# Kernel optimization log

Hardware: AMD Instinct MI355X
Metric: run time of the kernel (lower is better)

## Reference

```python
import jax, jax.numpy as jnp
import numpy as np

NEG = -1e9  # masked_fill value from the original
B, S, E, H, L, V, CTX = 4, 1024, 1024, 16, 12, 50257, 1024
D = E // H
PAD_IDX = 0


def layernorm(x, g, b, eps=1e-5):
    m = jnp.mean(x, axis=-1, keepdims=True)
    v = jnp.var(x, axis=-1, keepdims=True)
    return (x - m) * jax.lax.rsqrt(v + eps) * g + b


def setup_inputs() -> dict:
    key = jax.random.key(0)
    ks = jax.random.split(key, 8)
    sc = 0.02
    init = lambda k, shape: (jax.random.normal(k, shape, jnp.float32) * sc)
    return {
        "x": jax.random.randint(ks[0], (B, S), 0, V),
        "wte": init(ks[1], (V, E)),
        "wpe": init(ks[2], (CTX, E)),
        "Wq": init(ks[3], (L, E, E)), "bq": jnp.zeros((L, E), jnp.float32),
        "Wkv": init(ks[4], (L, E, E)), "bkv": jnp.zeros((L, E), jnp.float32),
        "Wfc": init(ks[5], (L, E, 4 * E)), "bfc": jnp.zeros((L, 4 * E), jnp.float32),
        "Wproj": init(ks[6], (L, 4 * E, E)), "bproj": jnp.zeros((L, E), jnp.float32),
        "ln1_g": jnp.ones((L, E), jnp.float32), "ln1_b": jnp.zeros((L, E), jnp.float32),
        "ln2_g": jnp.ones((L, E), jnp.float32), "ln2_b": jnp.zeros((L, E), jnp.float32),
        "lnf_g": jnp.ones((E,), jnp.float32), "lnf_b": jnp.zeros((E,), jnp.float32),
    }


def reference(x, wte, wpe, Wq, bq, Wkv, bkv, Wfc, bfc, Wproj, bproj,
              ln1_g, ln1_b, ln2_g, ln2_b, lnf_g, lnf_b):
    # key padding mask: mask = (x != pad_idx) broadcast over queries
    key_mask = (x != PAD_IDX)  # (B, S) over key positions
    h = wte[x] + wpe[:S]       # (B, S, E); dropout is identity in eval

    def block(h, p):
        wq, bq_, wkv, bkv_, wfc, bfc_, wpj, bpj, g1, b1, g2, b2 = p
        # Q = c_attn(x); K = V = c_proj(x)  (shared key/value tensor, as in source)
        q = (h @ wq + bq_).reshape(B, S, H, D)
        kv = (h @ wkv + bkv_).reshape(B, S, H, D)
        # unscaled QK^T (original applies no 1/sqrt(d) scaling)
        scores = jnp.einsum('blhd,bmhd->bhlm', q, kv)          # (B,H,S,S)
        scores = jnp.where(key_mask[:, None, None, :], scores, NEG)
        probs = jax.nn.softmax(scores, axis=-1)                # attn dropout = identity
        attn = jnp.einsum('bhlm,bmhd->blhd', probs, kv).reshape(B, S, E)
        u = layernorm(h + attn, g1, b1)                        # ln_1(x + attn)
        m = jax.nn.gelu(u @ wfc + bfc_, approximate=False) @ wpj + bpj
        # NOTE: second residual is the BLOCK INPUT h (not u), per the source
        return layernorm(m + h, g2, b2), None

    h, _ = jax.lax.scan(
        block, h,
        (Wq, bq, Wkv, bkv, Wfc, bfc, Wproj, bproj, ln1_g, ln1_b, ln2_g, ln2_b))
    return layernorm(h, lnf_g, lnf_b)
```

## Files before the change

### kernel.cpp

```cpp
#include <hip/hip_runtime.h>

#define SEQ    1024
#define EDIM   1024
#define NHEAD  16
#define DHEAD  64
#define NLAYER 12
#define NTOK   4096
#define QKVN   2048

typedef float f32x4  __attribute__((ext_vector_type(4)));
typedef short bf16x8 __attribute__((ext_vector_type(8)));

__device__ __forceinline__ unsigned short f32_to_bf16(float f) {
    union { float f; unsigned u; } v; v.f = f;
    return (unsigned short)((v.u + 0x7fffu + ((v.u >> 16) & 1u)) >> 16);
}
__device__ __forceinline__ float bf16_to_f32(unsigned short u) {
    union { unsigned u; float f; } v; v.u = (unsigned)u << 16;
    return v.f;
}

__device__ __forceinline__ float gelu_f(float x) {
    const float y = 0.7978845608028654f * (x + 0.044715f * x * x * x);
    const float e = __expf(-2.f * fabsf(y));
    float th = (1.f - e) / (1.f + e);
    th = (y < 0.f) ? -th : th;
    return 0.5f * x * (1.f + th);
}

__device__ __forceinline__ void gload_lds16(const unsigned short* g, unsigned short* l) {
    __builtin_amdgcn_global_load_lds((const __attribute__((address_space(1))) void*)g,
                                     (__attribute__((address_space(3))) void*)l, 16, 0, 0);
}

#define BARRIER() do { __builtin_amdgcn_s_barrier(); asm volatile("" ::: "memory"); } while (0)

__global__ __launch_bounds__(256) void transpose_bf16_k(
    const float* __restrict__ W, unsigned short* __restrict__ WT,
    int K, int N, size_t wStride, size_t wtStride)
{
    __shared__ float tile[32][33];
    const int l = blockIdx.z;
    W  += (size_t)l * wStride;
    WT += (size_t)l * wtStride;
    const int n0 = blockIdx.x * 32, k0 = blockIdx.y * 32;
    const int t = threadIdx.x;
    const int r = t >> 3, c4 = (t & 7) * 4;
    const float4 v = *reinterpret_cast<const float4*>(&W[(size_t)(k0 + r) * N + n0 + c4]);
    tile[r][c4 + 0] = v.x; tile[r][c4 + 1] = v.y;
    tile[r][c4 + 2] = v.z; tile[r][c4 + 3] = v.w;
    __syncthreads();
    ushort4 o;
    o.x = f32_to_bf16(tile[c4 + 0][r]);
    o.y = f32_to_bf16(tile[c4 + 1][r]);
    o.z = f32_to_bf16(tile[c4 + 2][r]);
    o.w = f32_to_bf16(tile[c4 + 3][r]);
    *reinterpret_cast<ushort4*>(&WT[(size_t)(n0 + r) * K + k0 + c4]) = o;
}

__global__ __launch_bounds__(256) void bias_concat_k(
    const float* __restrict__ bq, const float* __restrict__ bkv,
    float* __restrict__ bqkv)
{
    const int l = blockIdx.x, t = threadIdx.x;
    #pragma unroll
    for (int i = 0; i < 4; ++i) {
        const int c = t + i * 256;
        bqkv[(size_t)l * QKVN + c]        = bq[(size_t)l * EDIM + c];
        bqkv[(size_t)l * QKVN + EDIM + c] = bkv[(size_t)l * EDIM + c];
    }
}

__global__ __launch_bounds__(256) void embed_k(
    const int* __restrict__ x, const float* __restrict__ wte,
    const float* __restrict__ wpe, float* __restrict__ h,
    unsigned short* __restrict__ hb)
{
    const int bs  = blockIdx.x;
    const int s   = bs & (SEQ - 1);
    const int tok = x[bs];
    const int c   = threadIdx.x * 4;
    float4 a = *reinterpret_cast<const float4*>(&wte[(size_t)tok * EDIM + c]);
    const float4 p = *reinterpret_cast<const float4*>(&wpe[(size_t)s * EDIM + c]);
    a.x += p.x; a.y += p.y; a.z += p.z; a.w += p.w;
    *reinterpret_cast<float4*>(&h[(size_t)bs * EDIM + c]) = a;
    ushort4 o;
    o.x = f32_to_bf16(a.x); o.y = f32_to_bf16(a.y);
    o.z = f32_to_bf16(a.z); o.w = f32_to_bf16(a.w);
    *reinterpret_cast<ushort4*>(&hb[(size_t)bs * EDIM + c]) = o;
}

template<int WF32, int WBF16>
__global__ __launch_bounds__(256) void add_ln_k(
    const float* __restrict__ x1, const float* __restrict__ g,
    const float* __restrict__ b, float* __restrict__ outf,
    unsigned short* __restrict__ outb)
{
    const int row = blockIdx.x;
    const int t   = threadIdx.x;
    const int c   = t * 4;
    const size_t base = (size_t)row * EDIM + c;
    float4 a = *reinterpret_cast<const float4*>(x1 + base);
    float s  = a.x + a.y + a.z + a.w;
    float ss = a.x * a.x + a.y * a.y + a.z * a.z + a.w * a.w;
    #pragma unroll
    for (int o = 32; o > 0; o >>= 1) {
        s  += __shfl_down(s, o);
        ss += __shfl_down(ss, o);
    }
    __shared__ float rs[4], rss[4];
    const int lane = t & 63, wv = t >> 6;
    if (lane == 0) { rs[wv] = s; rss[wv] = ss; }
    __syncthreads();
    s  = rs[0] + rs[1] + rs[2] + rs[3];
    ss = rss[0] + rss[1] + rss[2] + rss[3];
    const float mean = s * (1.f / EDIM);
    const float var  = ss * (1.f / EDIM) - mean * mean;
    const float inv  = rsqrtf(var + 1e-5f);
    const float4 gv = *reinterpret_cast<const float4*>(g + c);
    const float4 bv = *reinterpret_cast<const float4*>(b + c);
    float4 y;
    y.x = (a.x - mean) * inv * gv.x + bv.x;
    y.y = (a.y - mean) * inv * gv.y + bv.y;
    y.z = (a.z - mean) * inv * gv.z + bv.z;
    y.w = (a.w - mean) * inv * gv.w + bv.w;
    if (WF32) *reinterpret_cast<float4*>(outf + base) = y;
    if (WBF16) {
        ushort4 o;
        o.x = f32_to_bf16(y.x); o.y = f32_to_bf16(y.y);
        o.z = f32_to_bf16(y.z); o.w = f32_to_bf16(y.w);
        *reinterpret_cast<ushort4*>(outb + base) = o;
    }
}

__global__ __launch_bounds__(256) void ln1_k(
    const float* __restrict__ h, const unsigned short* __restrict__ attb,
    const float* __restrict__ g, const float* __restrict__ b,
    unsigned short* __restrict__ ub)
{
    const int row = blockIdx.x;
    const int t   = threadIdx.x;
    const int c   = t * 4;
    const size_t base = (size_t)row * EDIM + c;
    float4 a = *reinterpret_cast<const float4*>(h + base);
    const ushort4 av = *reinterpret_cast<const ushort4*>(attb + base);
    a.x += bf16_to_f32(av.x); a.y += bf16_to_f32(av.y);
    a.z += bf16_to_f32(av.z); a.w += bf16_to_f32(av.w);
    float s  = a.x + a.y + a.z + a.w;
    float ss = a.x * a.x + a.y * a.y + a.z * a.z + a.w * a.w;
    #pragma unroll
    for (int o = 32; o > 0; o >>= 1) {
        s  += __shfl_down(s, o);
        ss += __shfl_down(ss, o);
    }
    __shared__ float rs[4], rss[4];
    const int lane = t & 63, wv = t >> 6;
    if (lane == 0) { rs[wv] = s; rss[wv] = ss; }
    __syncthreads();
    s  = rs[0] + rs[1] + rs[2] + rs[3];
    ss = rss[0] + rss[1] + rss[2] + rss[3];
    const float mean = s * (1.f / EDIM);
    const float var  = ss * (1.f / EDIM) - mean * mean;
    const float inv  = rsqrtf(var + 1e-5f);
    const float4 gv = *reinterpret_cast<const float4*>(g + c);
    const float4 bv = *reinterpret_cast<const float4*>(b + c);
    ushort4 o;
    o.x = f32_to_bf16((a.x - mean) * inv * gv.x + bv.x);
    o.y = f32_to_bf16((a.y - mean) * inv * gv.y + bv.y);
    o.z = f32_to_bf16((a.z - mean) * inv * gv.z + bv.z);
    o.w = f32_to_bf16((a.w - mean) * inv * gv.w + bv.w);
    *reinterpret_cast<ushort4*>(ub + base) = o;
}

__global__ __launch_bounds__(256) void ln2_k(
    const unsigned short* __restrict__ p0, const unsigned short* __restrict__ p1,
    const unsigned short* __restrict__ p2, const unsigned short* __restrict__ p3,
    const float* __restrict__ h, const float* __restrict__ g,
    const float* __restrict__ b, float* __restrict__ hout,
    unsigned short* __restrict__ hbout)
{
    const int row = blockIdx.x;
    const int t   = threadIdx.x;
    const int c   = t * 4;
    const size_t base = (size_t)row * EDIM + c;
    float4 a = *reinterpret_cast<const float4*>(h + base);
    const ushort4 v0 = *reinterpret_cast<const ushort4*>(p0 + base);
    const ushort4 v1 = *reinterpret_cast<const ushort4*>(p1 + base);
    const ushort4 v2 = *reinterpret_cast<const ushort4*>(p2 + base);
    const ushort4 v3 = *reinterpret_cast<const ushort4*>(p3 + base);
    a.x += bf16_to_f32(v0.x) + bf16_to_f32(v1.x) + bf16_to_f32(v2.x) + bf16_to_f32(v3.x);
    a.y += bf16_to_f32(v0.y) + bf16_to_f32(v1.y) + bf16_to_f32(v2.y) + bf16_to_f32(v3.y);
    a.z += bf16_to_f32(v0.z) + bf16_to_f32(v1.z) + bf16_to_f32(v2.z) + bf16_to_f32(v3.z);
    a.w += bf16_to_f32(v0.w) + bf16_to_f32(v1.w) + bf16_to_f32(v2.w) + bf16_to_f32(v3.w);
    float s  = a.x + a.y + a.z + a.w;
    float ss = a.x * a.x + a.y * a.y + a.z * a.z + a.w * a.w;
    #pragma unroll
    for (int o = 32; o > 0; o >>= 1) {
        s  += __shfl_down(s, o);
        ss += __shfl_down(ss, o);
    }
    __shared__ float rs[4], rss[4];
    const int lane = t & 63, wv = t >> 6;
    if (lane == 0) { rs[wv] = s; rss[wv] = ss; }
    __syncthreads();
    s  = rs[0] + rs[1] + rs[2] + rs[3];
    ss = rss[0] + rss[1] + rss[2] + rss[3];
    const float mean = s * (1.f / EDIM);
    const float var  = ss * (1.f / EDIM) - mean * mean;
    const float inv  = rsqrtf(var + 1e-5f);
    const float4 gv = *reinterpret_cast<const float4*>(g + c);
    const float4 bv = *reinterpret_cast<const float4*>(b + c);
    float4 y;
    y.x = (a.x - mean) * inv * gv.x + bv.x;
    y.y = (a.y - mean) * inv * gv.y + bv.y;
    y.z = (a.z - mean) * inv * gv.z + bv.z;
    y.w = (a.w - mean) * inv * gv.w + bv.w;
    *reinterpret_cast<float4*>(hout + base) = y;
    ushort4 o;
    o.x = f32_to_bf16(y.x); o.y = f32_to_bf16(y.y);
    o.z = f32_to_bf16(y.z); o.w = f32_to_bf16(y.w);
    *reinterpret_cast<ushort4*>(hbout + base) = o;
}

template<int GELU, int OUTBF16>
__global__ __launch_bounds__(256) void gemm_bt_k(
    const unsigned short* __restrict__ A,
    const unsigned short* __restrict__ BT,
    const float* __restrict__ bias, void* __restrict__ Cout,
    void* __restrict__ Cout2, int M, int N, int K)
{
    __shared__ unsigned short As[128 * 32];
    __shared__ unsigned short Bs[128 * 32];

    const int t    = threadIdx.x;
    const int lane = t & 63;
    const int wave = t >> 6;
    const int wr   = wave >> 1, wc = wave & 1;
    const int lrow = lane & 15, lgrp = lane >> 4;

    const int nbx = gridDim.x;
    int flat = blockIdx.y * nbx + blockIdx.x;
    const int nwg = nbx * gridDim.y;
    flat = (flat & 7) * (nwg >> 3) + (flat >> 3);
    const int row0 = (flat / nbx) * 128, col0 = (flat % nbx) * 128;

    const int kspan = K / gridDim.z;
    const int koff  = blockIdx.z * kspan;

    const int srow  = lane >> 2;
    const int skoff = (lane & 3) * 8;
    const unsigned short* aP0 = A  + (size_t)(row0 + 32 * wave + srow) * K + skoff;
    const unsigned short* aP1 = aP0 + (size_t)16 * K;
    const unsigned short* bP0 = BT + (size_t)(col0 + 32 * wave + srow) * K + skoff;
    const unsigned short* bP1 = bP0 + (size_t)16 * K;
    unsigned short* aL0 = As + wave * 1024;
    unsigned short* aL1 = As + wave * 1024 + 512;
    unsigned short* bL0 = Bs + wave * 1024;
    unsigned short* bL1 = Bs + wave * 1024 + 512;

    f32x4 acc[4][4];
    #pragma unroll
    for (int i = 0; i < 4; ++i)
        #pragma unroll
        for (int j = 0; j < 4; ++j)
            acc[i][j] = (f32x4){0.f, 0.f, 0.f, 0.f};

    for (int k0 = koff; k0 < koff + kspan; k0 += 32) {
        gload_lds16(aP0 + k0, aL0);
        gload_lds16(aP1 + k0, aL1);
        gload_lds16(bP0 + k0, bL0);
        gload_lds16(bP1 + k0, bL1);
        __syncthreads();

        bf16x8 af[4], bf[4];
        #pragma unroll
        for (int m = 0; m < 4; ++m)
            af[m] = *reinterpret_cast<const bf16x8*>(
                &As[(wr * 64 + m * 16 + lrow) * 32 + lgrp * 8]);
        #pragma unroll
        for (int n = 0; n < 4; ++n)
            bf[n] = *reinterpret_cast<const bf16x8*>(
                &Bs[(wc * 64 + n * 16 + lrow) * 32 + lgrp * 8]);

        #pragma unroll
        for (int n = 0; n < 4; ++n)
            #pragma unroll
            for (int m = 0; m < 4; ++m)
                acc[m][n] = __builtin_amdgcn_mfma_f32_16x16x32_bf16(
                    af[m], bf[n], acc[m][n], 0, 0, 0);
        __syncthreads();
    }

    const int z = blockIdx.z;
    #pragma unroll
    for (int n = 0; n < 4; ++n) {
        const int col = col0 + wc * 64 + n * 16 + lrow;
        const float bv = (z == 0) ? bias[col] : 0.f;
        #pragma unroll
        for (int m = 0; m < 4; ++m) {
            const int rb = row0 + wr * 64 + m * 16 + lgrp * 4;
            #pragma unroll
            for (int r = 0; r < 4; ++r) {
                float xv = acc[m][n][r] + bv;
                if (GELU) xv = gelu_f(xv);
                if (OUTBF16) {
                    ((unsigned short*)Cout)[(size_t)(rb + r) * N + col] = f32_to_bf16(xv);
                } else {
                    float* dst = (z == 0) ? (float*)Cout : (float*)Cout2;
                    dst[(size_t)(rb + r) * N + col] = xv;
                }
            }
        }
    }
}

template<int GELU, int OUT>
__global__ __launch_bounds__(512) void gemm256_k(
    const unsigned short* __restrict__ A,
    const unsigned short* __restrict__ BT,
    const float* __restrict__ bias, unsigned short* __restrict__ C,
    void* __restrict__ P0, void* __restrict__ P1,
    void* __restrict__ P2, void* __restrict__ P3,
    int M, int N, int K)
{
    __shared__ unsigned short sh[65536];
    unsigned short* Asm = sh;
    unsigned short* Bsm = sh + 32768;

    const int tid  = threadIdx.x;
    const int lane = tid & 63;
    const int wave = tid >> 6;
    const int wm   = wave >> 2;
    const int wn   = wave & 3;
    const int lrow = lane & 15, lgrp = lane >> 4;

    const int ntc = N >> 8;
    const int nwg = gridDim.x;
    int flat = (blockIdx.x & 7) * (nwg >> 3) + (blockIdx.x >> 3);
    const int row0 = (flat / ntc) * 256;
    const int col0 = (flat % ntc) * 256;

    const int kspan = K / gridDim.y;
    const int koff  = blockIdx.y * kspan;
    const int NT    = kspan >> 6;

    f32x4 acc[8][4];
    #pragma unroll
    for (int i = 0; i < 8; ++i)
        #pragma unroll
        for (int j = 0; j < 4; ++j)
            acc[i][j] = (f32x4){0.f, 0.f, 0.f, 0.f};

    auto stage_half = [&](const unsigned short* g, unsigned short* l) {
        #pragma unroll
        for (int c = 0; c < 2; ++c) {
            const int d = (tid + c * 512) * 16;
            const int L = d ^ (((d >> 7) & 7) << 4);
            gload_lds16(g + (size_t)(L >> 7) * K + ((L & 127) >> 1), l + (d >> 1));
        }
    };
    auto stageA = [&](int buf, int kt, int h) {
        stage_half(A + (size_t)(row0 + h * 128) * K + koff + kt * 64,
                   Asm + buf * 16384 + h * 8192);
    };
    auto stageB = [&](int buf, int kt, int h) {
        stage_half(BT + (size_t)(col0 + h * 128) * K + koff + kt * 64,
                   Bsm + buf * 16384 + h * 8192);
    };

    auto rdA = [&](int buf, int p, bf16x8 (&af)[2][2]) {
        #pragma unroll
        for (int m = 0; m < 2; ++m)
            #pragma unroll
            for (int ks = 0; ks < 2; ++ks) {
                const int r  = wm * 128 + p * 32 + m * 16 + lrow;
                const int cB = (ks * 64 + lgrp * 16) ^ ((r & 7) << 4);
                af[m][ks] = *reinterpret_cast<const bf16x8*>(
                    &Asm[buf * 16384 + ((r * 128 + cB) >> 1)]);
            }
    };
    auto rdB = [&](int buf, bf16x8 (&bfr)[4][2]) {
        #pragma unroll
        for (int n = 0; n < 4; ++n)
            #pragma unroll
            for (int ks = 0; ks < 2; ++ks) {
                const int r  = wn * 64 + n * 16 + lrow;
                const int cB = (ks * 64 + lgrp * 16) ^ ((r & 7) << 4);
                bfr[n][ks] = *reinterpret_cast<const bf16x8*>(
                    &Bsm[buf * 16384 + ((r * 128 + cB) >> 1)]);
            }
    };
    auto mq = [&](int p, bf16x8 (&af)[2][2], bf16x8 (&bfr)[4][2]) {
        __builtin_amdgcn_s_setprio(1);
        #pragma unroll
        for (int ks = 0; ks < 2; ++ks)
            #pragma unroll
            for (int n = 0; n < 4; ++n)
                #pragma unroll
                for (int m = 0; m < 2; ++m)
                    acc[p * 2 + m][n] = __builtin_amdgcn_mfma_f32_16x16x32_bf16(
                        af[m][ks], bfr[n][ks], acc[p * 2 + m][n], 0, 0, 0);
        __builtin_amdgcn_s_setprio(0);
    };

    stageA(0, 0, 0); stageA(0, 0, 1);
    stageB(0, 0, 0); stageB(0, 0, 1);
    stageA(1, 1, 0); stageA(1, 1, 1);
    stageB(1, 1, 0); stageB(1, 1, 1);
    asm volatile("s_waitcnt vmcnt(8)" ::: "memory");
    BARRIER();

    for (int t = 0; t < NT; t += 2) {
        bf16x8 bfr[4][2], af[2][2];
        rdB(0, bfr); rdA(0, 0, af);
        if (t > 0) { stageA(1, t + 1, 0); stageA(1, t + 1, 1); }
        BARRIER(); mq(0, af, bfr); BARRIER();
        rdA(0, 1, af);
        if (t + 2 < NT) stageB(0, t + 2, 0);
        BARRIER(); mq(1, af, bfr); BARRIER();
        rdA(0, 2, af);
        if (t + 2 < NT) stageB(0, t + 2, 1);
        BARRIER(); mq(2, af, bfr); BARRIER();
        rdA(0, 3, af);
        BARRIER(); mq(3, af, bfr);
        if (t + 2 < NT) { asm volatile("s_waitcnt vmcnt(4)" ::: "memory"); }
        else            { asm volatile("s_waitcnt vmcnt(0)" ::: "memory"); }
        BARRIER();
        rdB(1, bfr); rdA(1, 0, af);
        if (t + 2 < NT) stageA(0, t + 2, 0);
        BARRIER(); mq(0, af, bfr); BARRIER();
        rdA(1, 1, af);
        if (t + 2 < NT) stageA(0, t + 2, 1);
        if (t + 3 < NT) stageB(1, t + 3, 0);
        BARRIER(); mq(1, af, bfr); BARRIER();
        rdA(1, 2, af);
        if (t + 3 < NT) stageB(1, t + 3, 1);
        BARRIER(); mq(2, af, bfr); BARRIER();
        rdA(1, 3, af);
        BARRIER(); mq(3, af, bfr);
        if (t + 2 < NT) { asm volatile("s_waitcnt vmcnt(4)" ::: "memory"); }
        BARRIER();
    }

    const int z = blockIdx.y;
    #pragma unroll
    for (int n = 0; n < 4; ++n) {
        const int col = col0 + wn * 64 + n * 16 + lrow;
        const float bv = (z == 0) ? bias[col] : 0.f;
        #pragma unroll
        for (int mf = 0; mf < 8; ++mf) {
            const int rb = row0 + wm * 128 + mf * 16 + lgrp * 4;
            #pragma unroll
            for (int r = 0; r < 4; ++r) {
                float xv = acc[mf][n][r] + bv;
                if (GELU) xv = gelu_f(xv);
                if (OUT == 0) {
                    C[(size_t)(rb + r) * N + col] = f32_to_bf16(xv);
                } else {
                    unsigned short* dst = (unsigned short*)(
                        (z == 0) ? P0 : (z == 1) ? P1 : (z == 2) ? P2 : P3);
                    dst[(size_t)(rb + r) * N + col] = f32_to_bf16(xv);
                }
            }
        }
    }
}

#define KVP 68
__global__ __launch_bounds__(512) void attn_k(
    const unsigned short* __restrict__ qkv, const int* __restrict__ x,
    unsigned short* __restrict__ out)
{
    __shared__ unsigned short KVr[64][KVP];
    __shared__ unsigned short KVt[64 * 64];
    __shared__ unsigned short Ps[8][32][KVP];
    __shared__ float maskf[64];

    int flat = blockIdx.x + 4 * (blockIdx.y + 16 * blockIdx.z);
    flat = (flat & 7) * 32 + (flat >> 3);
    const int qt = flat & 3;
    const int hh = (flat >> 2) & 15;
    const int b  = flat >> 6;

    const int t    = threadIdx.x;
    const int w    = t >> 6;
    const int lane = t & 63;
    const int lrow = lane & 15, lgrp = lane >> 4;

    const unsigned short* qb_  = qkv + ((size_t)b * SEQ) * QKVN + hh * DHEAD;
    const unsigned short* kvb_ = qkv + ((size_t)b * SEQ) * QKVN + EDIM + hh * DHEAD;
    const int* xb = x + b * SEQ;
    const int qrow0 = qt * 256 + w * 32;

    bf16x8 qf[2][2];
    #pragma unroll
    for (int m = 0; m < 2; ++m)
        #pragma unroll
        for (int ks = 0; ks < 2; ++ks)
            qf[m][ks] = *reinterpret_cast<const bf16x8*>(
                qb_ + (size_t)(qrow0 + m * 16 + lrow) * QKVN + ks * 32 + lgrp * 8);

    f32x4 O[2][4];
    float mrun[2][4], lrun[2][4];
    #pragma unroll
    for (int m = 0; m < 2; ++m)
        #pragma unroll
        for (int i = 0; i < 4; ++i) {
            O[m][i] = (f32x4){0.f, 0.f, 0.f, 0.f};
            mrun[m][i] = -3e30f; lrun[m][i] = 0.f;
        }

    const int NKT = SEQ / 64;
    ushort4 kvreg[2];
    int xv = 0;

    auto issueKV = [&](int kt) {
        #pragma unroll
        for (int i = 0; i < 2; ++i) {
            const int u2 = t + i * 512;
            const int kr = u2 >> 4, kc = (u2 & 15) * 4;
            kvreg[i] = *reinterpret_cast<const ushort4*>(
                &kvb_[(size_t)(kt * 64 + kr) * QKVN + kc]);
        }
        if (t < 64) xv = xb[kt * 64 + t];
    };
    issueKV(0);

    for (int kt = 0; kt < NKT; ++kt) {
        __syncthreads();
        #pragma unroll
        for (int i = 0; i < 2; ++i) {
            const int u2 = t + i * 512;
            const int kr = u2 >> 4, kc = (u2 & 15) * 4;
            *reinterpret_cast<ushort4*>(&KVr[kr][kc]) = kvreg[i];
            const unsigned short comp[4] = {kvreg[i].x, kvreg[i].y, kvreg[i].z, kvreg[i].w};
            #pragma unroll
            for (int j = 0; j < 4; ++j) {
                const int d = kc + j;
                const int sw = (d ^ (d >> 3)) & 7;
                KVt[(d * 128 + ((kr * 2) ^ (sw << 4))) >> 1] = comp[j];
            }
        }
        if (t < 64) maskf[t] = (xv != 0) ? 1.f : 0.f;
        if (kt + 1 < NKT) issueKV(kt + 1);
        __syncthreads();

        f32x4 s[2][4];
        #pragma unroll
        for (int m = 0; m < 2; ++m)
            #pragma unroll
            for (int n = 0; n < 4; ++n) s[m][n] = (f32x4){0.f, 0.f, 0.f, 0.f};
        __builtin_amdgcn_s_setprio(1);
        #pragma unroll
        for (int ks = 0; ks < 2; ++ks)
            #pragma unroll
            for (int n = 0; n < 4; ++n) {
                union { bf16x8 v; ushort4 h[2]; } bb;
                bb.h[0] = *reinterpret_cast<const ushort4*>(
                    &KVr[16 * n + lrow][ks * 32 + lgrp * 8]);
                bb.h[1] = *reinterpret_cast<const ushort4*>(
                    &KVr[16 * n + lrow][ks * 32 + lgrp * 8 + 4]);
                #pragma unroll
                for (int m = 0; m < 2; ++m)
                    s[m][n] = __builtin_amdgcn_mfma_f32_16x16x32_bf16(
                        qf[m][ks], bb.v, s[m][n], 0, 0, 0);
            }
        __builtin_amdgcn_s_setprio(0);

        #pragma unroll
        for (int n = 0; n < 4; ++n) {
            const float flag = maskf[16 * n + lrow];
            #pragma unroll
            for (int m = 0; m < 2; ++m)
                #pragma unroll
                for (int r = 0; r < 4; ++r)
                    s[m][n][r] = (flag != 0.f) ? s[m][n][r] : -1e9f;
        }

        float tmax[2][4];
        float worst = -3e38f;
        #pragma unroll
        for (int m = 0; m < 2; ++m)
            #pragma unroll
            for (int r = 0; r < 4; ++r) {
                float v = fmaxf(fmaxf(s[m][0][r], s[m][1][r]),
                                fmaxf(s[m][2][r], s[m][3][r]));
                #pragma unroll
                for (int o = 1; o < 16; o <<= 1) v = fmaxf(v, __shfl_xor(v, o));
                tmax[m][r] = v;
                worst = fmaxf(worst, v - mrun[m][r]);
            }
        if (!__all(worst <= 8.f)) {
            #pragma unroll
            for (int m = 0; m < 2; ++m)
                #pragma unroll
                for (int r = 0; r < 4; ++r) {
                    const float mn = fmaxf(mrun[m][r], tmax[m][r]);
                    const float fs = __expf(mrun[m][r] - mn);
                    mrun[m][r] = mn;
                    lrun[m][r] *= fs;
                    #pragma unroll
                    for (int df = 0; df < 4; ++df) O[m][df][r] *= fs;
                }
        }

        #pragma unroll
        for (int m = 0; m < 2; ++m) {
            float rsum[4] = {0.f, 0.f, 0.f, 0.f};
            #pragma unroll
            for (int n = 0; n < 4; ++n)
                #pragma unroll
                for (int r = 0; r < 4; ++r) {
                    const float p = __expf(s[m][n][r] - mrun[m][r]);
                    rsum[r] += p;
                    Ps[w][m * 16 + 4 * lgrp + r][16 * n + lrow] = f32_to_bf16(p);
                }
            #pragma unroll
            for (int r = 0; r < 4; ++r) {
                float v = rsum[r];
                #pragma unroll
                for (int o = 1; o < 16; o <<= 1) v += __shfl_xor(v, o);
                lrun[m][r] += v;
            }
        }

        __builtin_amdgcn_s_setprio(1);
        #pragma unroll
        for (int ks = 0; ks < 2; ++ks) {
            bf16x8 paf[2];
            #pragma unroll
            for (int m = 0; m < 2; ++m) {
                union { bf16x8 v; ushort4 h[2]; } pp;
                pp.h[0] = *reinterpret_cast<const ushort4*>(
                    &Ps[w][m * 16 + lrow][ks * 32 + lgrp * 8]);
                pp.h[1] = *reinterpret_cast<const ushort4*>(
                    &Ps[w][m * 16 + lrow][ks * 32 + lgrp * 8 + 4]);
                paf[m] = pp.v;
            }
            #pragma unroll
            for (int df = 0; df < 4; ++df) {
                const int d  = 16 * df + lrow;
                const int sw = (d ^ (d >> 3)) & 7;
                const bf16x8 bvf = *reinterpret_cast<const bf16x8*>(
                    &KVt[(d * 128 + ((ks * 64 + lgrp * 16) ^ (sw << 4))) >> 1]);
                #pragma unroll
                for (int m = 0; m < 2; ++m)
                    O[m][df] = __builtin_amdgcn_mfma_f32_16x16x32_bf16(
                        paf[m], bvf, O[m][df], 0, 0, 0);
            }
        }
        __builtin_amdgcn_s_setprio(0);
    }

    #pragma unroll
    for (int m = 0; m < 2; ++m)
        #pragma unroll
        for (int r = 0; r < 4; ++r) {
            const float inv = 1.f / lrun[m][r];
            const int row = qrow0 + m * 16 + 4 * lgrp + r;
            unsigned short* po = out + ((size_t)b * SEQ + row) * EDIM + hh * DHEAD;
            #pragma unroll
            for (int df = 0; df < 4; ++df)
                po[16 * df + lrow] = f32_to_bf16(O[m][df][r] * inv);
        }
}

extern "C" void kernel_launch(void* const* d_in, const int* in_sizes, int n_in,
                              void* d_out, int out_size, void* d_ws, size_t ws_size,
                              hipStream_t stream)
{
    (void)in_sizes; (void)n_in; (void)out_size; (void)ws_size;

    const int*   x     = (const int*)  d_in[0];
    const float* wte   = (const float*)d_in[1];
    const float* wpe   = (const float*)d_in[2];
    const float* Wq    = (const float*)d_in[3];
    const float* bq    = (const float*)d_in[4];
    const float* Wkv   = (const float*)d_in[5];
    const float* bkv   = (const float*)d_in[6];
    const float* Wfc   = (const float*)d_in[7];
    const float* bfc   = (const float*)d_in[8];
    const float* Wproj = (const float*)d_in[9];
    const float* bproj = (const float*)d_in[10];
    const float* ln1g  = (const float*)d_in[11];
    const float* ln1b  = (const float*)d_in[12];
    const float* ln2g  = (const float*)d_in[13];
    const float* ln2b  = (const float*)d_in[14];
    const float* lnfg  = (const float*)d_in[15];
    const float* lnfb  = (const float*)d_in[16];

    const size_t MB = 1024 * 1024;
    char* W = (char*)d_ws;
    float*          h     = (float*)(W + 0 * MB);
    unsigned short* att   = (unsigned short*)(W + 16 * MB);
    unsigned short* pb0   = (unsigned short*)(W + 24 * MB);
    unsigned short* pb1   = (unsigned short*)(W + 32 * MB);
    unsigned short* pb2   = (unsigned short*)(W + 40 * MB);
    unsigned short* hb    = (unsigned short*)(W + 48 * MB);
    unsigned short* qkv   = (unsigned short*)(W + 56 * MB);
    unsigned short* pb3   = (unsigned short*)(W + 56 * MB);
    unsigned short* ub    = (unsigned short*)(W + 72 * MB);
    unsigned short* tb    = (unsigned short*)(W + 80 * MB);
    float*          bqkv  = (float*)(W + 112 * MB);
    unsigned short* wqkvT = (unsigned short*)(W + 113 * MB);
    unsigned short* wfcT  = (unsigned short*)(W + 161 * MB);
    unsigned short* wpjT  = (unsigned short*)(W + 257 * MB);

    bias_concat_k<<<NLAYER, 256, 0, stream>>>(bq, bkv, bqkv);
    transpose_bf16_k<<<dim3(32, 32, NLAYER), 256, 0, stream>>>(
        Wq, wqkvT, EDIM, EDIM, (size_t)EDIM * EDIM, (size_t)QKVN * EDIM);
    transpose_bf16_k<<<dim3(32, 32, NLAYER), 256, 0, stream>>>(
        Wkv, wqkvT + (size_t)EDIM * EDIM, EDIM, EDIM,
        (size_t)EDIM * EDIM, (size_t)QKVN * EDIM);
    transpose_bf16_k<<<dim3(128, 32, NLAYER), 256, 0, stream>>>(
        Wfc, wfcT, EDIM, 4 * EDIM, (size_t)4 * EDIM * EDIM, (size_t)4 * EDIM * EDIM);
    transpose_bf16_k<<<dim3(32, 128, NLAYER), 256, 0, stream>>>(
        Wproj, wpjT, 4 * EDIM, EDIM, (size_t)4 * EDIM * EDIM, (size_t)4 * EDIM * EDIM);

    embed_k<<<NTOK, 256, 0, stream>>>(x, wte, wpe, h, hb);

    for (int l = 0; l < NLAYER; ++l) {
        gemm_bt_k<0, 1><<<dim3(QKVN / 128, NTOK / 128), 256, 0, stream>>>(
            hb, wqkvT + (size_t)l * QKVN * EDIM, bqkv + (size_t)l * QKVN,
            qkv, nullptr, NTOK, QKVN, EDIM);

        attn_k<<<dim3(SEQ / 256, NHEAD, 4), 512, 0, stream>>>(qkv, x, att);

        ln1_k<<<NTOK, 256, 0, stream>>>(
            h, att, ln1g + l * EDIM, ln1b + l * EDIM, ub);

        gemm256_k<1, 0><<<dim3((NTOK / 256) * (4 * EDIM / 256), 1), 512, 0, stream>>>(
            ub, wfcT + (size_t)l * 4 * EDIM * EDIM, bfc + (size_t)l * 4 * EDIM,
            tb, nullptr, nullptr, nullptr, nullptr, NTOK, 4 * EDIM, EDIM);

        gemm256_k<0, 2><<<dim3((NTOK / 256) * (EDIM / 256), 4), 512, 0, stream>>>(
            tb, wpjT + (size_t)l * 4 * EDIM * EDIM, bproj + (size_t)l * EDIM,
            nullptr, pb0, pb1, pb2, pb3, NTOK, EDIM, 4 * EDIM);

        ln2_k<<<NTOK, 256, 0, stream>>>(
            pb0, pb1, pb2, pb3, h, ln2g + l * EDIM, ln2b + l * EDIM, h, hb);
    }

    add_ln_k<1, 0><<<NTOK, 256, 0, stream>>>(
        h, lnfg, lnfb, (float*)d_out, nullptr);
}
```

Baseline: 2.495 ms.

## Double attention KV tile to 128 and fold log2e into Q for exp2

The attention kernel now processes 128 keys per iteration instead of 64, so there are half as many barrier-separated iterations and fewer online-softmax rescales. Shared memory for K, its transpose and P grows to match. The QKV GEMM epilogue multiplies the Q columns by log2(e) so the softmax can use exp2f instead of __expf, and the lazy-rescale threshold is raised from 8 to 11 in the new base-2 units. The cost is more LDS and registers per block, which can reduce occupancy, and bf16 rounding now applies to the scaled Q values.

```diff
diff --git a/kernel.cpp b/kernel.cpp
--- a/kernel.cpp
+++ b/kernel.cpp
@@ -7,6 +7,7 @@
 #define NLAYER 12
 #define NTOK   4096
 #define QKVN   2048
+#define LOG2E  1.44269504088896f
 
 typedef float f32x4  __attribute__((ext_vector_type(4)));
 typedef short bf16x8 __attribute__((ext_vector_type(8)));
@@ -222,7 +223,7 @@
     *reinterpret_cast<ushort4*>(hbout + base) = o;
 }
 
-template<int GELU, int OUTBF16>
+template<int GELU, int OUTBF16, int QSCALE>
 __global__ __launch_bounds__(256) void gemm_bt_k(
     const unsigned short* __restrict__ A,
     const unsigned short* __restrict__ BT,
@@ -296,6 +297,7 @@
     for (int n = 0; n < 4; ++n) {
         const int col = col0 + wc * 64 + n * 16 + lrow;
         const float bv = (z == 0) ? bias[col] : 0.f;
+        const float qs = (QSCALE && col < EDIM) ? LOG2E : 1.f;
         #pragma unroll
         for (int m = 0; m < 4; ++m) {
             const int rb = row0 + wr * 64 + m * 16 + lgrp * 4;
@@ -303,6 +305,7 @@
             for (int r = 0; r < 4; ++r) {
                 float xv = acc[m][n][r] + bv;
                 if (GELU) xv = gelu_f(xv);
+                if (QSCALE) xv *= qs;
                 if (OUTBF16) {
                     ((unsigned short*)Cout)[(size_t)(rb + r) * N + col] = f32_to_bf16(xv);
                 } else {
@@ -466,15 +469,17 @@
     }
 }
 
+#define KVB 128
 #define KVP 68
+#define PSP 136
 __global__ __launch_bounds__(512) void attn_k(
     const unsigned short* __restrict__ qkv, const int* __restrict__ x,
     unsigned short* __restrict__ out)
 {
-    __shared__ unsigned short KVr[64][KVP];
-    __shared__ unsigned short KVt[64 * 64];
-    __shared__ unsigned short Ps[8][32][KVP];
-    __shared__ float maskf[64];
+    __shared__ unsigned short KVr[KVB][KVP];
+    __shared__ unsigned short KVt[64 * KVB];
+    __shared__ unsigned short Ps[8][32][PSP];
+    __shared__ float maskf[KVB];
 
     int flat = blockIdx.x + 4 * (blockIdx.y + 16 * blockIdx.z);
     flat = (flat & 7) * 32 + (flat >> 3);
@@ -510,26 +515,26 @@
             mrun[m][i] = -3e30f; lrun[m][i] = 0.f;
         }
 
-    const int NKT = SEQ / 64;
-    ushort4 kvreg[2];
+    const int NKT = SEQ / KVB;
+    ushort4 kvreg[4];
     int xv = 0;
 
     auto issueKV = [&](int kt) {
         #pragma unroll
-        for (int i = 0; i < 2; ++i) {
+        for (int i = 0; i < 4; ++i) {
             const int u2 = t + i * 512;
             const int kr = u2 >> 4, kc = (u2 & 15) * 4;
             kvreg[i] = *reinterpret_cast<const ushort4*>(
-                &kvb_[(size_t)(kt * 64 + kr) * QKVN + kc]);
-        }
-        if (t < 64) xv = xb[kt * 64 + t];
+                &kvb_[(size_t)(kt * KVB + kr) * QKVN + kc]);
+        }
+        if (t < KVB) xv = xb[kt * KVB + t];
     };
     issueKV(0);
 
     for (int kt = 0; kt < NKT; ++kt) {
         __syncthreads();
         #pragma unroll
-        for (int i = 0; i < 2; ++i) {
+        for (int i = 0; i < 4; ++i) {
             const int u2 = t + i * 512;
             const int kr = u2 >> 4, kc = (u2 & 15) * 4;
             *reinterpret_cast<ushort4*>(&KVr[kr][kc]) = kvreg[i];
@@ -538,23 +543,23 @@
             for (int j = 0; j < 4; ++j) {
                 const int d = kc + j;
                 const int sw = (d ^ (d >> 3)) & 7;
-                KVt[(d * 128 + ((kr * 2) ^ (sw << 4))) >> 1] = comp[j];
-            }
-        }
-        if (t < 64) maskf[t] = (xv != 0) ? 1.f : 0.f;
+                KVt[(d * 256 + ((kr * 2) ^ (sw << 4))) >> 1] = comp[j];
+            }
+        }
+        if (t < KVB) maskf[t] = (xv != 0) ? 1.f : 0.f;
         if (kt + 1 < NKT) issueKV(kt + 1);
         __syncthreads();
 
-        f32x4 s[2][4];
+        f32x4 s[2][8];
         #pragma unroll
         for (int m = 0; m < 2; ++m)
             #pragma unroll
-            for (int n = 0; n < 4; ++n) s[m][n] = (f32x4){0.f, 0.f, 0.f, 0.f};
+            for (int n = 0; n < 8; ++n) s[m][n] = (f32x4){0.f, 0.f, 0.f, 0.f};
         __builtin_amdgcn_s_setprio(1);
         #pragma unroll
         for (int ks = 0; ks < 2; ++ks)
             #pragma unroll
-            for (int n = 0; n < 4; ++n) {
+            for (int n = 0; n < 8; ++n) {
                 union { bf16x8 v; ushort4 h[2]; } bb;
                 bb.h[0] = *reinterpret_cast<const ushort4*>(
                     &KVr[16 * n + lrow][ks * 32 + lgrp * 8]);
@@ -568,7 +573,7 @@
         __builtin_amdgcn_s_setprio(0);
 
         #pragma unroll
-        for (int n = 0; n < 4; ++n) {
+        for (int n = 0; n < 8; ++n) {
             const float flag = maskf[16 * n + lrow];
             #pragma unroll
             for (int m = 0; m < 2; ++m)
@@ -583,20 +588,22 @@
         for (int m = 0; m < 2; ++m)
             #pragma unroll
             for (int r = 0; r < 4; ++r) {
-                float v = fmaxf(fmaxf(s[m][0][r], s[m][1][r]),
-                                fmaxf(s[m][2][r], s[m][3][r]));
+                float v = fmaxf(fmaxf(fmaxf(s[m][0][r], s[m][1][r]),
+                                      fmaxf(s[m][2][r], s[m][3][r])),
+                                fmaxf(fmaxf(s[m][4][r], s[m][5][r]),
+                                      fmaxf(s[m][6][r], s[m][7][r])));
                 #pragma unroll
                 for (int o = 1; o < 16; o <<= 1) v = fmaxf(v, __shfl_xor(v, o));
                 tmax[m][r] = v;
                 worst = fmaxf(worst, v - mrun[m][r]);
             }
-        if (!__all(worst <= 8.f)) {
+        if (!__all(worst <= 11.f)) {
             #pragma unroll
             for (int m = 0; m < 2; ++m)
                 #pragma unroll
                 for (int r = 0; r < 4; ++r) {
                     const float mn = fmaxf(mrun[m][r], tmax[m][r]);
-                    const float fs = __expf(mrun[m][r] - mn);
+                    const float fs = exp2f(mrun[m][r] - mn);
                     mrun[m][r] = mn;
                     lrun[m][r] *= fs;
                     #pragma unroll
@@ -608,10 +615,10 @@
         for (int m = 0; m < 2; ++m) {
             float rsum[4] = {0.f, 0.f, 0.f, 0.f};
             #pragma unroll
-            for (int n = 0; n < 4; ++n)
+            for (int n = 0; n < 8; ++n)
                 #pragma unroll
                 for (int r = 0; r < 4; ++r) {
-                    const float p = __expf(s[m][n][r] - mrun[m][r]);
+                    const float p = exp2f(s[m][n][r] - mrun[m][r]);
                     rsum[r] += p;
                     Ps[w][m * 16 + 4 * lgrp + r][16 * n + lrow] = f32_to_bf16(p);
                 }
@@ -626,15 +633,15 @@
 
         __builtin_amdgcn_s_setprio(1);
         #pragma unroll
-        for (int ks = 0; ks < 2; ++ks) {
+        for (int ks2 = 0; ks2 < 4; ++ks2) {
             bf16x8 paf[2];
             #pragma unroll
             for (int m = 0; m < 2; ++m) {
                 union { bf16x8 v; ushort4 h[2]; } pp;
                 pp.h[0] = *reinterpret_cast<const ushort4*>(
-                    &Ps[w][m * 16 + lrow][ks * 32 + lgrp * 8]);
+                    &Ps[w][m * 16 + lrow][ks2 * 32 + lgrp * 8]);
                 pp.h[1] = *reinterpret_cast<const ushort4*>(
-                    &Ps[w][m * 16 + lrow][ks * 32 + lgrp * 8 + 4]);
+                    &Ps[w][m * 16 + lrow][ks2 * 32 + lgrp * 8 + 4]);
                 paf[m] = pp.v;
             }
             #pragma unroll
@@ -642,7 +649,7 @@
                 const int d  = 16 * df + lrow;
                 const int sw = (d ^ (d >> 3)) & 7;
                 const bf16x8 bvf = *reinterpret_cast<const bf16x8*>(
-                    &KVt[(d * 128 + ((ks * 64 + lgrp * 16) ^ (sw << 4))) >> 1]);
+                    &KVt[(d * 256 + ((ks2 * 64 + lgrp * 16) ^ (sw << 4))) >> 1]);
                 #pragma unroll
                 for (int m = 0; m < 2; ++m)
                     O[m][df] = __builtin_amdgcn_mfma_f32_16x16x32_bf16(
@@ -720,7 +727,7 @@
     embed_k<<<NTOK, 256, 0, stream>>>(x, wte, wpe, h, hb);
 
     for (int l = 0; l < NLAYER; ++l) {
-        gemm_bt_k<0, 1><<<dim3(QKVN / 128, NTOK / 128), 256, 0, stream>>>(
+        gemm_bt_k<0, 1, 1><<<dim3(QKVN / 128, NTOK / 128), 256, 0, stream>>>(
             hb, wqkvT + (size_t)l * QKVN * EDIM, bqkv + (size_t)l * QKVN,
             qkv, nullptr, NTOK, QKVN, EDIM);
 
```

After: 2.457 ms. Within noise of the previous version (-1.5%).
